# Kernel tuning notes

Hardware: AMD Instinct MI355X
Metric: run time of the kernel (lower is better)

## Reference

```python
import jax, jax.numpy as jnp
import numpy as np

HID = 256


def setup_inputs() -> dict:
    key0 = jax.random.key(0)
    ks = jax.random.split(key0, 6)
    bsz, m, Lq, Lk = 8, 16, 64, 2048
    query = jax.random.normal(ks[0], (bsz, Lq, HID), dtype=jnp.float32)
    key = jax.random.normal(ks[1], (bsz * m, Lk, HID), dtype=jnp.float32)
    # nn.Linear params (weight is [out, in]); init scale ~ 1/sqrt(fan_in)
    s = 1.0 / np.sqrt(HID)
    w_q = jax.random.uniform(ks[2], (HID, HID), jnp.float32, -s, s)
    b_q = jax.random.uniform(ks[3], (HID,), jnp.float32, -s, s)
    w_k = jax.random.uniform(ks[4], (HID, HID), jnp.float32, -s, s)
    b_k = jax.random.uniform(ks[5], (HID,), jnp.float32, -s, s)
    return {"query": query, "key": key, "w_q": w_q, "b_q": b_q, "w_k": w_k, "b_k": b_k}


def reference(query, key, w_q, b_q, w_k, b_k):
    bsz = query.shape[0]
    msz = key.shape[0]
    m = msz // bsz
    hid = query.shape[-1]
    scale = jnp.sqrt(jnp.float32(hid))
    Q = jnp.einsum("bqh,oh->bqo", query, w_q) + b_q            # [b, Lq, h]
    K = jnp.einsum("nkh,oh->nko", key, w_k) + b_k              # [b*m, Lk, h]
    K = K.reshape(bsz, m, -1, hid)                               # [b, m, Lk, h]
    key_r = key.reshape(bsz, m, -1, hid)                         # [b, m, Lk, h]
    # energy[b,m,q,k] = Q[b,q,:] . K[b,m,k,:] / sqrt(hid)
    energy = jnp.einsum("bqh,bmkh->bmqk", Q, K) / scale         # [b, m, Lq, Lk]
    total_attention = jnp.sum(energy, axis=-2)                   # [b, m, Lk]
    attention = jnp.mean(total_attention, axis=-1)               # [b, m]
    max_index = jnp.argmax(attention, axis=-1)                   # [b]
    # gather the raw key block for the best candidate per batch item
    val = jnp.take_along_axis(key_r, max_index[:, None, None, None], axis=1)
    return val[:, 0]                                             # [b, Lk, h]
```

## Files before the change

### kernel.cpp

```cpp
#include <hip/hip_runtime.h>

#define HID 256
#define LK  2048
#define LQ  64
#define BSZ 8
#define M   16
#define NKEY (BSZ * M)

__global__ void colsum_kernel(const float* __restrict__ query,
                              const float* __restrict__ key,
                              const float* __restrict__ w_q,
                              const float* __restrict__ b_q,
                              const float* __restrict__ w_k,
                              float* __restrict__ partial,
                              float* __restrict__ u,
                              unsigned long long* __restrict__ amax,
                              int split) {
    const int bid  = blockIdx.x;
    const int t    = threadIdx.x;
    const int wave = t >> 6;
    const int lane = t & 63;

    if (bid < BSZ) {
        if (t == 0) amax[bid] = 0ull;
        __shared__ float qs[HID];
        __shared__ float qsv[HID];
        const int b = bid;
        const float* qbase = query + (size_t)b * LQ * HID;
        float s = 0.f;
        for (int r = 0; r < LQ; ++r) s += qbase[(size_t)r * HID + t];
        qs[t] = s;
        __syncthreads();
        const float4* wrow = (const float4*)(w_q + (size_t)t * HID);
        float acc = 0.f;
#pragma unroll 8
        for (int h4 = 0; h4 < HID / 4; ++h4) {
            float4 w = wrow[h4];
            acc += w.x * qs[h4 * 4 + 0] + w.y * qs[h4 * 4 + 1]
                 + w.z * qs[h4 * 4 + 2] + w.w * qs[h4 * 4 + 3];
        }
        qsv[t] = acc + (float)LQ * b_q[t];
        __syncthreads();
        float uh = 0.f;
#pragma unroll 4
        for (int o = 0; o < HID; ++o) uh += qsv[o] * w_k[(size_t)o * HID + t];
        u[(size_t)b * HID + t] = uh;
    } else {
        const int kb    = bid - BSZ;
        const int n     = kb / split;
        const int chunk = kb % split;
        const int rows  = LK / split;
        const float* base = key + (size_t)n * LK * HID + (size_t)chunk * rows * HID;

        const int rpw = rows / 4;
        const int r0  = wave * rpw;
        float4 a0 = make_float4(0.f, 0.f, 0.f, 0.f);
        float4 a1 = make_float4(0.f, 0.f, 0.f, 0.f);
        float4 a2 = make_float4(0.f, 0.f, 0.f, 0.f);
        float4 a3 = make_float4(0.f, 0.f, 0.f, 0.f);
#pragma unroll 4
        for (int i = 0; i < rpw; i += 4) {
            float4 v0 = ((const float4*)(base + (size_t)(r0 + i + 0) * HID))[lane];
            float4 v1 = ((const float4*)(base + (size_t)(r0 + i + 1) * HID))[lane];
            float4 v2 = ((const float4*)(base + (size_t)(r0 + i + 2) * HID))[lane];
            float4 v3 = ((const float4*)(base + (size_t)(r0 + i + 3) * HID))[lane];
            a0.x += v0.x; a0.y += v0.y; a0.z += v0.z; a0.w += v0.w;
            a1.x += v1.x; a1.y += v1.y; a1.z += v1.z; a1.w += v1.w;
            a2.x += v2.x; a2.y += v2.y; a2.z += v2.z; a2.w += v2.w;
            a3.x += v3.x; a3.y += v3.y; a3.z += v3.z; a3.w += v3.w;
        }
        a0.x = (a0.x + a1.x) + (a2.x + a3.x);
        a0.y = (a0.y + a1.y) + (a2.y + a3.y);
        a0.z = (a0.z + a1.z) + (a2.z + a3.z);
        a0.w = (a0.w + a1.w) + (a2.w + a3.w);

        __shared__ float lds[4][HID];
        ((float4*)lds[wave])[lane] = a0;
        __syncthreads();
        partial[(size_t)kb * HID + t] =
            (lds[0][t] + lds[1][t]) + (lds[2][t] + lds[3][t]);
    }
}

__global__ void att_kernel(const float* __restrict__ partial,
                           const float* __restrict__ u,
                           unsigned long long* __restrict__ amax,
                           int split) {
    const int n    = blockIdx.x;
    const int b    = n / M;
    const int m    = n % M;
    const int t    = threadIdx.x;
    const int wave = t >> 6;
    const int lane = t & 63;

    const float* p = partial + (size_t)n * split * HID + t;
    float s0 = 0.f, s1 = 0.f, s2 = 0.f, s3 = 0.f;
    int c = 0;
    for (; c + 4 <= split; c += 4) {
        s0 += p[(size_t)(c + 0) * HID];
        s1 += p[(size_t)(c + 1) * HID];
        s2 += p[(size_t)(c + 2) * HID];
        s3 += p[(size_t)(c + 3) * HID];
    }
    for (; c < split; ++c) s0 += p[(size_t)c * HID];

    float v = ((s0 + s1) + (s2 + s3)) * u[(size_t)b * HID + t];
    for (int off = 32; off; off >>= 1) v += __shfl_down(v, off);

    __shared__ float wp[4];
    if (lane == 0) wp[wave] = v;
    __syncthreads();
    if (t == 0) {
        float att = (wp[0] + wp[1]) + (wp[2] + wp[3]);
        unsigned int fb = __float_as_uint(att);
        unsigned int mono = (fb & 0x80000000u) ? ~fb : (fb | 0x80000000u);
        unsigned long long pack =
            ((unsigned long long)mono << 32) | (unsigned int)(M - 1 - m);
        atomicMax(&amax[b], pack);
    }
}

__global__ void gather_kernel(const float* __restrict__ key,
                              const unsigned long long* __restrict__ amax,
                              float* __restrict__ out) {
    const int b = blockIdx.y;
    const unsigned long long v = amax[b];
    const int m = M - 1 - (int)(v & 0xFFFFFFFFu);
    const int n = b * M + m;
    const size_t per_b = (size_t)LK * HID / 4;
    const size_t off = (size_t)blockIdx.x * blockDim.x + threadIdx.x;
    ((float4*)out)[(size_t)b * per_b + off] =
        ((const float4*)key)[(size_t)n * per_b + off];
}

extern "C" void kernel_launch(void* const* d_in, const int* in_sizes, int n_in,
                              void* d_out, int out_size, void* d_ws, size_t ws_size,
                              hipStream_t stream) {
    const float* query = (const float*)d_in[0];
    const float* key   = (const float*)d_in[1];
    const float* w_q   = (const float*)d_in[2];
    const float* b_q   = (const float*)d_in[3];
    const float* w_k   = (const float*)d_in[4];
    float* out = (float*)d_out;

    int split = 32;
    while (split > 1) {
        size_t need = sizeof(unsigned long long) * BSZ
                      + sizeof(float) * ((size_t)NKEY * split * HID
                                         + (size_t)BSZ * HID);
        if (need <= ws_size) break;
        split >>= 1;
    }

    unsigned long long* amax = (unsigned long long*)d_ws;
    float* partial = (float*)(amax + BSZ);
    float* u       = partial + (size_t)NKEY * split * HID;

    hipLaunchKernelGGL(colsum_kernel, dim3(BSZ + NKEY * split), dim3(256), 0,
                       stream, query, key, w_q, b_q, w_k, partial, u, amax, split);

    hipLaunchKernelGGL(att_kernel, dim3(NKEY), dim3(256), 0, stream,
                       partial, u, amax, split);

    hipLaunchKernelGGL(gather_kernel, dim3(512, BSZ), dim3(256), 0, stream,
                       key, amax, out);
}
```

Baseline: 69.81 us.

## Fix key split to 8 and parallelize query-side projection across waves

Replaces the workspace-dependent split of 32 with a compile-time split of 8, so each key-summing block reduces 256 rows and the number of blocks and partial sums shrinks. The per-batch query blocks now sum query rows and compute the w_k projection using float4 loads spread across four waves with an LDS reduction, replacing serial per-thread loops with strided scalar loads. The partial-sum reduction in att_kernel is fully unrolled. The main risk is fewer blocks in flight (1032) for the memory-bound key scan, though each block does more work.

```diff
diff --git a/kernel.cpp b/kernel.cpp
--- a/kernel.cpp
+++ b/kernel.cpp
@@ -6,6 +6,7 @@
 #define BSZ 8
 #define M   16
 #define NKEY (BSZ * M)
+#define SPLIT 8
 
 __global__ void colsum_kernel(const float* __restrict__ query,
                               const float* __restrict__ key,
@@ -14,8 +15,7 @@
                               const float* __restrict__ w_k,
                               float* __restrict__ partial,
                               float* __restrict__ u,
-                              unsigned long long* __restrict__ amax,
-                              int split) {
+                              unsigned long long* __restrict__ amax) {
     const int bid  = blockIdx.x;
     const int t    = threadIdx.x;
     const int wave = t >> 6;
@@ -23,17 +23,26 @@
 
     if (bid < BSZ) {
         if (t == 0) amax[bid] = 0ull;
+        __shared__ float lds[4][HID];
         __shared__ float qs[HID];
         __shared__ float qsv[HID];
         const int b = bid;
         const float* qbase = query + (size_t)b * LQ * HID;
-        float s = 0.f;
-        for (int r = 0; r < LQ; ++r) s += qbase[(size_t)r * HID + t];
-        qs[t] = s;
+
+        float4 a = make_float4(0.f, 0.f, 0.f, 0.f);
+#pragma unroll
+        for (int r = 0; r < LQ / 4; ++r) {
+            float4 v = ((const float4*)(qbase + (size_t)(wave * (LQ / 4) + r) * HID))[lane];
+            a.x += v.x; a.y += v.y; a.z += v.z; a.w += v.w;
+        }
+        ((float4*)lds[wave])[lane] = a;
         __syncthreads();
+        qs[t] = (lds[0][t] + lds[1][t]) + (lds[2][t] + lds[3][t]);
+        __syncthreads();
+
         const float4* wrow = (const float4*)(w_q + (size_t)t * HID);
         float acc = 0.f;
-#pragma unroll 8
+#pragma unroll
         for (int h4 = 0; h4 < HID / 4; ++h4) {
             float4 w = wrow[h4];
             acc += w.x * qs[h4 * 4 + 0] + w.y * qs[h4 * 4 + 1]
@@ -41,15 +50,23 @@
         }
         qsv[t] = acc + (float)LQ * b_q[t];
         __syncthreads();
-        float uh = 0.f;
-#pragma unroll 4
-        for (int o = 0; o < HID; ++o) uh += qsv[o] * w_k[(size_t)o * HID + t];
-        u[(size_t)b * HID + t] = uh;
+
+        float4 ua = make_float4(0.f, 0.f, 0.f, 0.f);
+#pragma unroll 8
+        for (int i = 0; i < 64; ++i) {
+            const int o = wave * 64 + i;
+            float4 w = ((const float4*)(w_k + (size_t)o * HID))[lane];
+            const float q = qsv[o];
+            ua.x += q * w.x; ua.y += q * w.y; ua.z += q * w.z; ua.w += q * w.w;
+        }
+        ((float4*)lds[wave])[lane] = ua;
+        __syncthreads();
+        u[(size_t)b * HID + t] = (lds[0][t] + lds[1][t]) + (lds[2][t] + lds[3][t]);
     } else {
         const int kb    = bid - BSZ;
-        const int n     = kb / split;
-        const int chunk = kb % split;
-        const int rows  = LK / split;
+        const int n     = kb / SPLIT;
+        const int chunk = kb % SPLIT;
+        const int rows  = LK / SPLIT;
         const float* base = key + (size_t)n * LK * HID + (size_t)chunk * rows * HID;
 
         const int rpw = rows / 4;
@@ -74,18 +91,17 @@
         a0.z = (a0.z + a1.z) + (a2.z + a3.z);
         a0.w = (a0.w + a1.w) + (a2.w + a3.w);
 
-        __shared__ float lds[4][HID];
-        ((float4*)lds[wave])[lane] = a0;
+        __shared__ float klds[4][HID];
+        ((float4*)klds[wave])[lane] = a0;
         __syncthreads();
         partial[(size_t)kb * HID + t] =
-            (lds[0][t] + lds[1][t]) + (lds[2][t] + lds[3][t]);
+            (klds[0][t] + klds[1][t]) + (klds[2][t] + klds[3][t]);
     }
 }
 
 __global__ void att_kernel(const float* __restrict__ partial,
                            const float* __restrict__ u,
-                           unsigned long long* __restrict__ amax,
-                           int split) {
+                           unsigned long long* __restrict__ amax) {
     const int n    = blockIdx.x;
     const int b    = n / M;
     const int m    = n % M;
@@ -93,18 +109,15 @@
     const int wave = t >> 6;
     const int lane = t & 63;
 
-    const float* p = partial + (size_t)n * split * HID + t;
-    float s0 = 0.f, s1 = 0.f, s2 = 0.f, s3 = 0.f;
-    int c = 0;
-    for (; c + 4 <= split; c += 4) {
-        s0 += p[(size_t)(c + 0) * HID];
-        s1 += p[(size_t)(c + 1) * HID];
-        s2 += p[(size_t)(c + 2) * HID];
-        s3 += p[(size_t)(c + 3) * HID];
-    }
-    for (; c < split; ++c) s0 += p[(size_t)c * HID];
+    const float* p = partial + (size_t)n * SPLIT * HID + t;
+    float s = 0.f;
+    float sv[SPLIT];
+#pragma unroll
+    for (int c = 0; c < SPLIT; ++c) sv[c] = p[(size_t)c * HID];
+#pragma unroll
+    for (int c = 0; c < SPLIT; ++c) s += sv[c];
 
-    float v = ((s0 + s1) + (s2 + s3)) * u[(size_t)b * HID + t];
+    float v = s * u[(size_t)b * HID + t];
     for (int off = 32; off; off >>= 1) v += __shfl_down(v, off);
 
     __shared__ float wp[4];
@@ -143,24 +156,15 @@
     const float* w_k   = (const float*)d_in[4];
     float* out = (float*)d_out;
 
-    int split = 32;
-    while (split > 1) {
-        size_t need = sizeof(unsigned long long) * BSZ
-                      + sizeof(float) * ((size_t)NKEY * split * HID
-                                         + (size_t)BSZ * HID);
-        if (need <= ws_size) break;
-        split >>= 1;
-    }
-
     unsigned long long* amax = (unsigned long long*)d_ws;
     float* partial = (float*)(amax + BSZ);
-    float* u       = partial + (size_t)NKEY * split * HID;
+    float* u       = partial + (size_t)NKEY * SPLIT * HID;
 
-    hipLaunchKernelGGL(colsum_kernel, dim3(BSZ + NKEY * split), dim3(256), 0,
-                       stream, query, key, w_q, b_q, w_k, partial, u, amax, split);
+    hipLaunchKernelGGL(colsum_kernel, dim3(BSZ + NKEY * SPLIT), dim3(256), 0,
+                       stream, query, key, w_q, b_q, w_k, partial, u, amax);
 
     hipLaunchKernelGGL(att_kernel, dim3(NKEY), dim3(256), 0, stream,
-                       partial, u, amax, split);
+                       partial, u, amax);
 
     hipLaunchKernelGGL(gather_kernel, dim3(512, BSZ), dim3(256), 0, stream,
                        key, amax, out);
```

After: 74.72 us. 1.07x slower.
